# Optimization experiments

Measured on AMD Instinct MI355X. Metric: run time of the kernel, lower is better.

Reference implementation:

```python
import jax, jax.numpy as jnp
import numpy as np

DIM = 256
RES = 64
SPLIT = 8
HEADS = 8
H_SP, W_SP = RES, SPLIT  # idx = 0 -> horizontal strips
HD = DIM // HEADS
SCALE = HD ** (-0.5)
WIN = H_SP * W_SP  # 512 tokens per window


def _to_windows(x, B, H, W, C):
    x = x.reshape(B, H // H_SP, H_SP, W // W_SP, W_SP, C)
    x = x.transpose(0, 1, 3, 2, 4, 5).reshape(-1, WIN, HEADS, HD)
    return x.transpose(0, 2, 1, 3)


def setup_inputs() -> dict:
    key = jax.random.key(0)
    k1, k2, k3 = jax.random.split(key, 3)
    qkv = jax.random.normal(k1, (3, 4, RES * RES, DIM), dtype=jnp.float32)
    conv_w = jax.random.normal(k2, (DIM, 1, 3, 3), dtype=jnp.float32) * 0.1
    conv_b = jax.random.normal(k3, (DIM,), dtype=jnp.float32) * 0.01
    return {"qkv": qkv, "conv_w": conv_w, "conv_b": conv_b}


def reference(qkv, conv_w, conv_b):
    q, k, v = qkv[0], qkv[1], qkv[2]
    B, L, C = q.shape
    H = W = RES
    qw = _to_windows(q, B, H, W, C) * SCALE
    kw = _to_windows(k, B, H, W, C)
    # v as per-window images [nWB, C, H_SP, W_SP] for depthwise LePE conv
    vimg = v.reshape(B, H // H_SP, H_SP, W // W_SP, W_SP, C)
    vimg = vimg.transpose(0, 1, 3, 5, 2, 4).reshape(-1, C, H_SP, W_SP)
    lepe = jax.lax.conv_general_dilated(
        vimg, conv_w, window_strides=(1, 1), padding='SAME',
        feature_group_count=C,
        dimension_numbers=('NCHW', 'OIHW', 'NCHW')) + conv_b[None, :, None, None]
    vw = vimg.reshape(-1, HEADS, HD, WIN).transpose(0, 1, 3, 2)
    lepe = lepe.reshape(-1, HEADS, HD, WIN).transpose(0, 1, 3, 2)
    attn = jax.nn.softmax(jnp.einsum('whqd,whkd->whqk', qw, kw), axis=-1)
    x = jnp.einsum('whqk,whkd->whqd', attn, vw) + lepe
    # windows -> image -> tokens (matches windows2img)
    x = x.transpose(0, 2, 1, 3).reshape(-1, WIN, C)
    x = x.reshape(B, H // H_SP, W // W_SP, H_SP, W_SP, C)
    x = x.transpose(0, 1, 3, 2, 4, 5).reshape(B, H * W, C)
    return x, attn
```

## Files before the change

kernel.cpp:

```cpp
#include <hip/hip_runtime.h>
#include <hip/hip_bf16.h>

typedef __attribute__((ext_vector_type(8))) __bf16 bf16x8;
typedef __attribute__((ext_vector_type(4))) float f32x4;


__global__ __launch_bounds__(256, 1)
void lepe_attn(const float* __restrict__ qkv,
               const float* __restrict__ conv_w,
               const float* __restrict__ conv_b,
               float* __restrict__ out)
{
    constexpr int kL = 4096, kC = 256, kHD = 32;
    constexpr int KSTR = 40;
    constexpr int VSTR = 520;
    constexpr int PSTR = 520;

    __shared__ __align__(16) __bf16 sK [512 * KSTR];
    __shared__ __align__(16) __bf16 sVt[ 32 * VSTR];
    __shared__ __align__(16) __bf16 sP [4 * 16 * PSTR];

    const int bx = blockIdx.x;
    const int wb = bx >> 3;
    const int h  = bx & 7;
    const int b  = wb >> 3;
    const int w  = wb & 7;
    const int tid  = threadIdx.x;
    const int lane = tid & 63;
    const int wave = tid >> 6;
    const int l15  = lane & 15;
    const int quad = lane >> 4;

    const float* kBase = qkv + (size_t)4 * kL * kC;
    const float* vBase = qkv + (size_t)8 * kL * kC;

    #pragma unroll
    for (int chunk = 0; chunk < 8; ++chunk) {
        int e  = chunk * 2048 + tid * 8;
        int t  = e >> 5;
        int d0 = e & 31;
        int l  = ((t >> 3) << 6) + (w << 3) + (t & 7);
        size_t g = ((size_t)(b * kL + l)) * kC + h * kHD + d0;
        f32x4 k0 = *(const f32x4*)(kBase + g);
        f32x4 k1 = *(const f32x4*)(kBase + g + 4);
        bf16x8 kk;
        kk[0] = (__bf16)k0[0]; kk[1] = (__bf16)k0[1];
        kk[2] = (__bf16)k0[2]; kk[3] = (__bf16)k0[3];
        kk[4] = (__bf16)k1[0]; kk[5] = (__bf16)k1[1];
        kk[6] = (__bf16)k1[2]; kk[7] = (__bf16)k1[3];
        *(bf16x8*)&sK[t * KSTR + d0] = kk;
        f32x4 v0 = *(const f32x4*)(vBase + g);
        f32x4 v1 = *(const f32x4*)(vBase + g + 4);
        sVt[(d0 + 0) * VSTR + t] = (__bf16)v0[0];
        sVt[(d0 + 1) * VSTR + t] = (__bf16)v0[1];
        sVt[(d0 + 2) * VSTR + t] = (__bf16)v0[2];
        sVt[(d0 + 3) * VSTR + t] = (__bf16)v0[3];
        sVt[(d0 + 4) * VSTR + t] = (__bf16)v1[0];
        sVt[(d0 + 5) * VSTR + t] = (__bf16)v1[1];
        sVt[(d0 + 6) * VSTR + t] = (__bf16)v1[2];
        sVt[(d0 + 7) * VSTR + t] = (__bf16)v1[3];
    }

    float w9[2][9], wbias[2];
    #pragma unroll
    for (int nt = 0; nt < 2; ++nt) {
        int c = h * kHD + nt * 16 + l15;
        #pragma unroll
        for (int k = 0; k < 9; ++k) w9[nt][k] = conv_w[c * 9 + k];
        wbias[nt] = conv_b[c];
    }

    __syncthreads();

    float* attnOut = out + (size_t)4 * kL * kC;
    __bf16* sPw = &sP[wave * 16 * PSTR];

    for (int qt = 0; qt < 8; ++qt) {
        const int qrow0 = qt * 64 + wave * 16;

        int tq = qrow0 + l15;
        int lq = ((tq >> 3) << 6) + (w << 3) + (tq & 7);
        const float* qp = qkv + ((size_t)(b * kL + lq)) * kC + h * kHD + quad * 8;
        f32x4 q0 = *(const f32x4*)qp;
        f32x4 q1 = *(const f32x4*)(qp + 4);
        bf16x8 a_frag;
        a_frag[0] = (__bf16)q0[0]; a_frag[1] = (__bf16)q0[1];
        a_frag[2] = (__bf16)q0[2]; a_frag[3] = (__bf16)q0[3];
        a_frag[4] = (__bf16)q1[0]; a_frag[5] = (__bf16)q1[1];
        a_frag[6] = (__bf16)q1[2]; a_frag[7] = (__bf16)q1[3];

        f32x4 accS[32];
        const f32x4 zf = {0.f, 0.f, 0.f, 0.f};
        #pragma unroll
        for (int nt = 0; nt < 32; ++nt) {
            bf16x8 b_frag = *(const bf16x8*)&sK[(nt * 16 + l15) * KSTR + quad * 8];
            accS[nt] = __builtin_amdgcn_mfma_f32_16x16x32_bf16(a_frag, b_frag, zf, 0, 0, 0);
        }

        float mr[4] = {-3.0e38f, -3.0e38f, -3.0e38f, -3.0e38f};
        #pragma unroll
        for (int nt = 0; nt < 32; ++nt) {
            #pragma unroll
            for (int r = 0; r < 4; ++r) {
                float sv = accS[nt][r] * 0.17677669529663687f;
                accS[nt][r] = sv;
                mr[r] = fmaxf(mr[r], sv);
            }
        }
        #pragma unroll
        for (int r = 0; r < 4; ++r) {
            mr[r] = fmaxf(mr[r], __shfl_xor(mr[r], 1));
            mr[r] = fmaxf(mr[r], __shfl_xor(mr[r], 2));
            mr[r] = fmaxf(mr[r], __shfl_xor(mr[r], 4));
            mr[r] = fmaxf(mr[r], __shfl_xor(mr[r], 8));
        }
        float sr[4] = {0.f, 0.f, 0.f, 0.f};
        #pragma unroll
        for (int nt = 0; nt < 32; ++nt) {
            #pragma unroll
            for (int r = 0; r < 4; ++r) {
                float e = __expf(accS[nt][r] - mr[r]);
                accS[nt][r] = e;
                sr[r] += e;
            }
        }
        float inv[4];
        #pragma unroll
        for (int r = 0; r < 4; ++r) {
            sr[r] += __shfl_xor(sr[r], 1);
            sr[r] += __shfl_xor(sr[r], 2);
            sr[r] += __shfl_xor(sr[r], 4);
            sr[r] += __shfl_xor(sr[r], 8);
            inv[r] = 1.0f / sr[r];
        }

        const size_t attnRowBase = (size_t)bx * 512 * 512 + (size_t)(qrow0 + quad * 4) * 512;
        #pragma unroll
        for (int nt = 0; nt < 32; ++nt) {
            int col = nt * 16 + l15;
            #pragma unroll
            for (int r = 0; r < 4; ++r) {
                float p = accS[nt][r] * inv[r];
                attnOut[attnRowBase + (size_t)r * 512 + col] = p;
                sPw[(quad * 4 + r) * PSTR + col] = (__bf16)p;
            }
        }

        f32x4 accO0 = {0.f, 0.f, 0.f, 0.f}, accO1 = {0.f, 0.f, 0.f, 0.f};
        #pragma unroll
        for (int kt = 0; kt < 16; ++kt) {
            bf16x8 pa  = *(const bf16x8*)&sPw[l15 * PSTR + kt * 32 + quad * 8];
            bf16x8 vb0 = *(const bf16x8*)&sVt[ l15        * VSTR + kt * 32 + quad * 8];
            bf16x8 vb1 = *(const bf16x8*)&sVt[(16 + l15) * VSTR + kt * 32 + quad * 8];
            accO0 = __builtin_amdgcn_mfma_f32_16x16x32_bf16(pa, vb0, accO0, 0, 0, 0);
            accO1 = __builtin_amdgcn_mfma_f32_16x16x32_bf16(pa, vb1, accO1, 0, 0, 0);
        }

        const int t0  = qrow0 + quad * 4;
        const int r0  = t0 >> 3;
        const int cw0 = t0 & 7;
        #pragma unroll
        for (int nt = 0; nt < 2; ++nt) {
            const int dch = nt * 16 + l15;
            float patch[3][6];
            #pragma unroll
            for (int i = 0; i < 3; ++i) {
                int r2 = r0 - 1 + i;
                #pragma unroll
                for (int j = 0; j < 6; ++j) {
                    int c2 = cw0 - 1 + j;
                    bool ok = (r2 >= 0) && (r2 < 64) && (c2 >= 0) && (c2 < 8);
                    patch[i][j] = ok ? (float)sVt[dch * VSTR + r2 * 8 + c2] : 0.0f;
                }
            }
            #pragma unroll
            for (int r = 0; r < 4; ++r) {
                float acc = (nt ? accO1[r] : accO0[r]) + wbias[nt];
                #pragma unroll
                for (int i = 0; i < 3; ++i)
                    #pragma unroll
                    for (int jj = 0; jj < 3; ++jj)
                        acc += w9[nt][i * 3 + jj] * patch[i][r + jj];
                int trow = t0 + r;
                int lo = ((trow >> 3) << 6) + (w << 3) + (trow & 7);
                out[((size_t)(b * kL + lo)) * kC + h * kHD + dch] = acc;
            }
        }
    }
}

extern "C" void kernel_launch(void* const* d_in, const int* in_sizes, int n_in,
                              void* d_out, int out_size, void* d_ws, size_t ws_size,
                              hipStream_t stream) {
    const float* qkv = (const float*)d_in[0];
    const float* cw  = (const float*)d_in[1];
    const float* cb  = (const float*)d_in[2];
    float* outp = (float*)d_out;
    lepe_attn<<<dim3(256), dim3(256), 0, stream>>>(qkv, cw, cb, outp);
}
```

Baseline: 338.7 us.

## Coalesce attention-probability stores, defer softmax normalization, and use eight waves per block

The attention matrix is now written as contiguous float4 vectors, rebuilt from the bf16 P tile in shared memory, instead of scattered scalar stores. Softmax uses exp2 with a folded scale, and normalization is applied after the PV matmul. Blocks double to 512 threads, each processing 128 query rows per iteration with a half-width P buffer. The stored probabilities now carry bf16 rounding, and the 128-register limit from the launch bounds may force spills of the 32-tile score accumulator.

Result: slower. 347.5 us (+2.6%).

```diff
diff --git a/kernel.cpp b/kernel.cpp
--- a/kernel.cpp
+++ b/kernel.cpp
@@ -5,7 +5,9 @@
 typedef __attribute__((ext_vector_type(4))) float f32x4;
 
 
-__global__ __launch_bounds__(256, 1)
+#define S2F 0.2550633201964024f
+
+__global__ __launch_bounds__(512, 2)
 void lepe_attn(const float* __restrict__ qkv,
                const float* __restrict__ conv_w,
                const float* __restrict__ conv_b,
@@ -14,11 +16,11 @@
     constexpr int kL = 4096, kC = 256, kHD = 32;
     constexpr int KSTR = 40;
     constexpr int VSTR = 520;
-    constexpr int PSTR = 520;
+    constexpr int PSTR = 264;
 
     __shared__ __align__(16) __bf16 sK [512 * KSTR];
     __shared__ __align__(16) __bf16 sVt[ 32 * VSTR];
-    __shared__ __align__(16) __bf16 sP [4 * 16 * PSTR];
+    __shared__ __align__(16) __bf16 sP [8 * 16 * PSTR];
 
     const int bx = blockIdx.x;
     const int wb = bx >> 3;
@@ -35,8 +37,8 @@
     const float* vBase = qkv + (size_t)8 * kL * kC;
 
     #pragma unroll
-    for (int chunk = 0; chunk < 8; ++chunk) {
-        int e  = chunk * 2048 + tid * 8;
+    for (int chunk = 0; chunk < 4; ++chunk) {
+        int e  = chunk * 4096 + tid * 8;
         int t  = e >> 5;
         int d0 = e & 31;
         int l  = ((t >> 3) << 6) + (w << 3) + (t & 7);
@@ -75,8 +77,8 @@
     float* attnOut = out + (size_t)4 * kL * kC;
     __bf16* sPw = &sP[wave * 16 * PSTR];
 
-    for (int qt = 0; qt < 8; ++qt) {
-        const int qrow0 = qt * 64 + wave * 16;
+    for (int qt = 0; qt < 4; ++qt) {
+        const int qrow0 = qt * 128 + wave * 16;
 
         int tq = qrow0 + l15;
         int lq = ((tq >> 3) << 6) + (w << 3) + (tq & 7);
@@ -102,7 +104,7 @@
         for (int nt = 0; nt < 32; ++nt) {
             #pragma unroll
             for (int r = 0; r < 4; ++r) {
-                float sv = accS[nt][r] * 0.17677669529663687f;
+                float sv = accS[nt][r] * S2F;
                 accS[nt][r] = sv;
                 mr[r] = fmaxf(mr[r], sv);
             }
@@ -119,7 +121,7 @@
         for (int nt = 0; nt < 32; ++nt) {
             #pragma unroll
             for (int r = 0; r < 4; ++r) {
-                float e = __expf(accS[nt][r] - mr[r]);
+                float e = exp2f(accS[nt][r] - mr[r]);
                 accS[nt][r] = e;
                 sr[r] += e;
             }
@@ -134,26 +136,37 @@
             inv[r] = 1.0f / sr[r];
         }
 
-        const size_t attnRowBase = (size_t)bx * 512 * 512 + (size_t)(qrow0 + quad * 4) * 512;
-        #pragma unroll
-        for (int nt = 0; nt < 32; ++nt) {
-            int col = nt * 16 + l15;
-            #pragma unroll
-            for (int r = 0; r < 4; ++r) {
-                float p = accS[nt][r] * inv[r];
-                attnOut[attnRowBase + (size_t)r * 512 + col] = p;
-                sPw[(quad * 4 + r) * PSTR + col] = (__bf16)p;
-            }
-        }
-
-        f32x4 accO0 = {0.f, 0.f, 0.f, 0.f}, accO1 = {0.f, 0.f, 0.f, 0.f};
-        #pragma unroll
-        for (int kt = 0; kt < 16; ++kt) {
-            bf16x8 pa  = *(const bf16x8*)&sPw[l15 * PSTR + kt * 32 + quad * 8];
-            bf16x8 vb0 = *(const bf16x8*)&sVt[ l15        * VSTR + kt * 32 + quad * 8];
-            bf16x8 vb1 = *(const bf16x8*)&sVt[(16 + l15) * VSTR + kt * 32 + quad * 8];
-            accO0 = __builtin_amdgcn_mfma_f32_16x16x32_bf16(pa, vb0, accO0, 0, 0, 0);
-            accO1 = __builtin_amdgcn_mfma_f32_16x16x32_bf16(pa, vb1, accO1, 0, 0, 0);
+        const float invL = inv[(lane >> 2) & 3];
+        const size_t aBase = (size_t)bx * (512 * 512)
+                           + (size_t)(qrow0 + (lane >> 2)) * 512 + (lane & 3) * 8;
+
+        f32x4 accO0 = zf, accO1 = zf;
+        #pragma unroll
+        for (int half = 0; half < 2; ++half) {
+            #pragma unroll
+            for (int nt = 0; nt < 16; ++nt) {
+                #pragma unroll
+                for (int r = 0; r < 4; ++r)
+                    sPw[(quad * 4 + r) * PSTR + nt * 16 + l15] =
+                        (__bf16)accS[half * 16 + nt][r];
+            }
+            #pragma unroll
+            for (int c = 0; c < 8; ++c) {
+                bf16x8 pa  = *(const bf16x8*)&sPw[l15 * PSTR + c * 32 + quad * 8];
+                bf16x8 vb0 = *(const bf16x8*)&sVt[ l15        * VSTR + half * 256 + c * 32 + quad * 8];
+                bf16x8 vb1 = *(const bf16x8*)&sVt[(16 + l15) * VSTR + half * 256 + c * 32 + quad * 8];
+                accO0 = __builtin_amdgcn_mfma_f32_16x16x32_bf16(pa, vb0, accO0, 0, 0, 0);
+                accO1 = __builtin_amdgcn_mfma_f32_16x16x32_bf16(pa, vb1, accO1, 0, 0, 0);
+                bf16x8 ee = *(const bf16x8*)&sPw[(lane >> 2) * PSTR + c * 32 + (lane & 3) * 8];
+                f32x4 o0, o1;
+                #pragma unroll
+                for (int j = 0; j < 4; ++j) {
+                    o0[j] = (float)ee[j] * invL;
+                    o1[j] = (float)ee[4 + j] * invL;
+                }
+                *(f32x4*)(attnOut + aBase + half * 256 + c * 32)     = o0;
+                *(f32x4*)(attnOut + aBase + half * 256 + c * 32 + 4) = o1;
+            }
         }
 
         const int t0  = qrow0 + quad * 4;
@@ -175,7 +188,7 @@
             }
             #pragma unroll
             for (int r = 0; r < 4; ++r) {
-                float acc = (nt ? accO1[r] : accO0[r]) + wbias[nt];
+                float acc = (nt ? accO1[r] : accO0[r]) * inv[r] + wbias[nt];
                 #pragma unroll
                 for (int i = 0; i < 3; ++i)
                     #pragma unroll
@@ -196,5 +209,5 @@
     const float* cw  = (const float*)d_in[1];
     const float* cb  = (const float*)d_in[2];
     float* outp = (float*)d_out;
-    lepe_attn<<<dim3(256), dim3(256), 0, stream>>>(qkv, cw, cb, outp);
+    lepe_attn<<<dim3(256), dim3(512), 0, stream>>>(qkv, cw, cb, outp);
 }
```
